# Optimization experiments

Hardware: AMD Instinct MI355X
Metric: run time of the kernel (lower is better)

Reference implementation:

```python
import jax, jax.numpy as jnp
import numpy as np

ALPHA = 0.5
PATH_LEN = 7  # 1 start entity + 3 (module, entity) hops
NUM_ENTITIES = 200000
EMBED = 128
NUM_MOD = 64
HIDDEN = 512
OUT_DIM = 64
BATCH = 8192


def setup_inputs() -> dict:
    key = jax.random.key(0)
    ks = jax.random.split(key, 8)
    stdv = 1.0 / np.sqrt(EMBED)
    return {
        "entity_embeds": jax.random.normal(ks[0], (NUM_ENTITIES, EMBED), jnp.float32) * 0.05,
        "W_mods": jax.random.uniform(ks[1], (NUM_MOD, EMBED, EMBED), jnp.float32, -stdv, stdv),
        "W1": jax.random.normal(ks[2], (HIDDEN, EMBED), jnp.float32) * stdv,
        "b1": jax.random.normal(ks[3], (HIDDEN,), jnp.float32) * 0.01,
        "W2": jax.random.normal(ks[4], (OUT_DIM, HIDDEN), jnp.float32) * (1.0 / np.sqrt(HIDDEN)),
        "b2": jax.random.normal(ks[5], (OUT_DIM,), jnp.float32) * 0.01,
        "entity_ids": jax.random.randint(ks[6], (BATCH, 4), 0, NUM_ENTITIES, jnp.int64 if jax.config.jax_enable_x64 else jnp.int32),
        "module_ids": jax.random.randint(ks[7], (BATCH, 3), 0, NUM_MOD, jnp.int64 if jax.config.jax_enable_x64 else jnp.int32),
    }


def reference(entity_embeds, W_mods, W1, b1, W2, b2, entity_ids, module_ids):
    # Batched version of ModuleNet.forward over a batch of fixed-length-7 paths.
    x = entity_embeds[entity_ids[:, 0]]  # [B, E] start entity embedding
    bias = x
    for h in range(3):  # hops over (module_id, entity_id) pairs
        Wm = W_mods[module_ids[:, h]]          # [B, E, E] per-row weight gather
        bias = entity_embeds[entity_ids[:, h + 1]]  # [B, E]
        x = jax.nn.relu(jnp.einsum('boi,bi->bo', Wm, x) + bias)
    w = 1.0 / (PATH_LEN * ALPHA)
    out = (1.0 - w) * bias + w * x  # [B, E]
    # classifier: Linear -> ReLU -> Linear
    h1 = jax.nn.relu(out @ W1.T + b1)
    logits = h1 @ W2.T + b2  # [B, OUT_DIM]
    return logits
```

## Files before the change

kernel.cpp:

```cpp
#include <hip/hip_runtime.h>

namespace {

typedef short bf16x8 __attribute__((ext_vector_type(8)));
typedef float f32x4 __attribute__((ext_vector_type(4)));

constexpr int BATCH = 8192;
constexpr int NMOD  = 64;
constexpr int CAP   = 256;
constexpr int CSTR  = 16;
constexpr float WB  = 1.0f / (7.0f * 0.5f);

constexpr size_t OFF_WHI = 0;
constexpr size_t OFF_WLO = 524288;
constexpr size_t OFF_XH0 = 1048576;
constexpr size_t OFF_XL0 = 1572864;
constexpr size_t OFF_XH1 = 2097152;
constexpr size_t OFF_XL1 = 2621440;
constexpr size_t OFF_W1H = 3145728;
constexpr size_t OFF_W1L = 3178496;
constexpr size_t OFF_W2H = 3211264;
constexpr size_t OFF_W2L = 3227648;
constexpr size_t OFF_CNT = 3244032;
constexpr size_t OFF_BKT = 3247104;

__device__ __forceinline__ ushort f2bf(float x) {
  unsigned u = __builtin_bit_cast(unsigned, x);
  u += 0x7FFFu + ((u >> 16) & 1u);
  return (ushort)(u >> 16);
}
__device__ __forceinline__ float bf2f(ushort h) {
  return __builtin_bit_cast(float, ((unsigned)h) << 16);
}
__device__ __forceinline__ void cvt8(const float* v, bf16x8& hi, bf16x8& lo) {
#pragma unroll
  for (int j = 0; j < 8; ++j) {
    const float x = v[j];
    const ushort h = f2bf(x);
    hi[j] = (short)h;
    lo[j] = (short)f2bf(x - bf2f(h));
  }
}

__global__ __launch_bounds__(256) void k_prep(const float* __restrict__ Wm,
                                              const float* __restrict__ W1,
                                              const float* __restrict__ W2,
                                              const int* __restrict__ mids,
                                              float* __restrict__ ws) {
  const int bx = blockIdx.x;
  const int tid = threadIdx.x;
  if (bx < 560) {
    const float* src;
    ushort *dh, *dl;
    size_t i8;
    if (bx < 512) {
      src = Wm; dh = (ushort*)(ws + OFF_WHI); dl = (ushort*)(ws + OFF_WLO);
      i8 = (size_t)bx * 256 + tid;
    } else if (bx < 544) {
      src = W1; dh = (ushort*)(ws + OFF_W1H); dl = (ushort*)(ws + OFF_W1L);
      i8 = (size_t)(bx - 512) * 256 + tid;
    } else {
      src = W2; dh = (ushort*)(ws + OFF_W2H); dl = (ushort*)(ws + OFF_W2L);
      i8 = (size_t)(bx - 544) * 256 + tid;
    }
    float v[8];
    *(float4*)&v[0] = *(const float4*)&src[i8 * 8];
    *(float4*)&v[4] = *(const float4*)&src[i8 * 8 + 4];
    bf16x8 hi, lo;
    cvt8(v, hi, lo);
    *(bf16x8*)&dh[i8 * 8] = hi;
    *(bf16x8*)&dl[i8 * 8] = lo;
  } else {
    const int idx = (bx - 560) * 256 + tid;
    if (idx < BATCH * 3) {
      const int b = idx / 3, h = idx - b * 3;
      const int m = mids[idx];
      int* cnt = (int*)(ws + OFF_CNT);
      int* bkt = (int*)(ws + OFF_BKT);
      const int pos = atomicAdd(&cnt[(h * NMOD + m) * CSTR], 1);
      bkt[(h * NMOD + m) * CAP + pos] = b;
    }
  }
}

template <int HOP>
__global__ __launch_bounds__(256, 2) void k_hop(const float* __restrict__ E,
                                                const int* __restrict__ eids,
                                                float* __restrict__ ws) {
  const int m = blockIdx.x >> 2, sl = blockIdx.x & 3;
  const int cn = ((const int*)(ws + OFF_CNT))[(HOP * NMOD + m) * CSTR];
  const int r0 = sl * 64;
  if (r0 >= cn) return;
  const int nr = min(64, cn - r0);

  __shared__ ushort wh[128 * 72];
  __shared__ ushort wl[128 * 72];
  __shared__ int rows[64], esrc[64], ebia[64];

  const int tid = threadIdx.x;
  const ushort* WhiG = (const ushort*)(ws + OFF_WHI) + (size_t)m * 16384;
  const ushort* WloG = (const ushort*)(ws + OFF_WLO) + (size_t)m * 16384;
  const int* bkt = (const int*)(ws + OFF_BKT) + (HOP * NMOD + m) * CAP + r0;
  const ushort* XHp = (const ushort*)(ws + (HOP == 2 ? OFF_XH1 : OFF_XH0));
  const ushort* XLp = (const ushort*)(ws + (HOP == 2 ? OFF_XL1 : OFF_XL0));
  ushort* XHn = (ushort*)(ws + (HOP == 1 ? OFF_XH1 : OFF_XH0));
  ushort* XLn = (ushort*)(ws + (HOP == 1 ? OFF_XL1 : OFF_XL0));

  if (tid < 64) {
    const int b = bkt[tid < nr ? tid : 0];
    rows[tid] = b;
    esrc[tid] = (HOP == 0) ? eids[b * 4] : b;
    ebia[tid] = eids[b * 4 + HOP + 1];
  }

  const int w = tid >> 6, l = tid & 63;
  const int lg = l >> 4, lr = l & 15;
  const int g0 = (w & 1) * 2, f0 = (w >> 1) * 4;

  f32x4 acc[2][4] = {};

#pragma unroll
  for (int p = 0; p < 2; ++p) {
    __syncthreads();
    for (int e = tid; e < 128 * 8; e += 256) {
      const int c = e >> 3, s = e & 7;
      *(bf16x8*)&wh[c * 72 + s * 8] =
          *(const bf16x8*)&WhiG[(size_t)c * 128 + p * 64 + s * 8];
      *(bf16x8*)&wl[c * 72 + s * 8] =
          *(const bf16x8*)&WloG[(size_t)c * 128 + p * 64 + s * 8];
    }
    __syncthreads();

    bf16x8 ah[2][2], al[2][2];
#pragma unroll
    for (int g = 0; g < 2; ++g) {
      const int row = (g0 + g) * 16 + lr;
#pragma unroll
      for (int s = 0; s < 2; ++s) {
        const int k0 = p * 64 + s * 32 + lg * 8;
        if (HOP == 0) {
          const float* sp = E + (size_t)esrc[row] * 128;
          float v[8];
          *(float4*)&v[0] = *(const float4*)&sp[k0];
          *(float4*)&v[4] = *(const float4*)&sp[k0 + 4];
          cvt8(v, ah[g][s], al[g][s]);
        } else {
          const size_t xo = (size_t)esrc[row] * 128 + k0;
          ah[g][s] = *(const bf16x8*)&XHp[xo];
          al[g][s] = *(const bf16x8*)&XLp[xo];
        }
      }
    }

#pragma unroll
    for (int f = 0; f < 4; ++f) {
      const int c = (f0 + f) * 16 + lr;
      bf16x8 bh[2], bl[2];
#pragma unroll
      for (int s = 0; s < 2; ++s) {
        bh[s] = *(const bf16x8*)&wh[c * 72 + s * 32 + lg * 8];
        bl[s] = *(const bf16x8*)&wl[c * 72 + s * 32 + lg * 8];
      }
#pragma unroll
      for (int g = 0; g < 2; ++g) {
#pragma unroll
        for (int s = 0; s < 2; ++s) {
          acc[g][f] = __builtin_amdgcn_mfma_f32_16x16x32_bf16(
              ah[g][s], bh[s], acc[g][f], 0, 0, 0);
          acc[g][f] = __builtin_amdgcn_mfma_f32_16x16x32_bf16(
              al[g][s], bh[s], acc[g][f], 0, 0, 0);
          acc[g][f] = __builtin_amdgcn_mfma_f32_16x16x32_bf16(
              ah[g][s], bl[s], acc[g][f], 0, 0, 0);
        }
      }
    }
  }

#pragma unroll
  for (int g = 0; g < 2; ++g) {
#pragma unroll
    for (int q = 0; q < 4; ++q) {
      const int row = (g0 + g) * 16 + lg * 4 + q;
      if (row < nr) {
        const int b = rows[row];
        const float* bp = E + (size_t)ebia[row] * 128;
        const size_t ob = (size_t)b * 128;
#pragma unroll
        for (int f = 0; f < 4; ++f) {
          const int col = (f0 + f) * 16 + lr;
          const float bias = bp[col];
          float v = fmaxf(acc[g][f][q] + bias, 0.f);
          if (HOP == 2) v = (1.f - WB) * bias + WB * v;
          const ushort h = f2bf(v);
          XHn[ob + col] = h;
          XLn[ob + col] = f2bf(v - bf2f(h));
        }
      }
    }
  }
}

constexpr int HSTR = 520;
__global__ __launch_bounds__(256, 2) void k_mlp(const float* __restrict__ b1,
                                                const float* __restrict__ b2,
                                                float* __restrict__ ws,
                                                float* __restrict__ out) {
  __shared__ ushort hh[16 * HSTR];
  __shared__ ushort hl[16 * HSTR];
  const int tid = threadIdx.x;
  const int row0 = blockIdx.x * 16;
  const ushort* XH = (const ushort*)(ws + OFF_XH0);
  const ushort* XL = (const ushort*)(ws + OFF_XL0);
  const ushort* W1H = (const ushort*)(ws + OFF_W1H);
  const ushort* W1L = (const ushort*)(ws + OFF_W1L);
  const ushort* W2H = (const ushort*)(ws + OFF_W2H);
  const ushort* W2L = (const ushort*)(ws + OFF_W2L);

  const int w = tid >> 6, l = tid & 63;
  const int lg = l >> 4, lr = l & 15;

  bf16x8 ah[4], al[4];
#pragma unroll
  for (int s = 0; s < 4; ++s) {
    const size_t xo = (size_t)(row0 + lr) * 128 + s * 32 + lg * 8;
    ah[s] = *(const bf16x8*)&XH[xo];
    al[s] = *(const bf16x8*)&XL[xo];
  }
  f32x4 acc[8] = {};
#pragma unroll
  for (int f = 0; f < 8; ++f) {
    const int c = w * 128 + f * 16 + lr;
#pragma unroll
    for (int s = 0; s < 4; ++s) {
      const size_t wo = (size_t)c * 128 + s * 32 + lg * 8;
      const bf16x8 bh = *(const bf16x8*)&W1H[wo];
      const bf16x8 bl = *(const bf16x8*)&W1L[wo];
      acc[f] = __builtin_amdgcn_mfma_f32_16x16x32_bf16(ah[s], bh, acc[f], 0, 0, 0);
      acc[f] = __builtin_amdgcn_mfma_f32_16x16x32_bf16(al[s], bh, acc[f], 0, 0, 0);
      acc[f] = __builtin_amdgcn_mfma_f32_16x16x32_bf16(ah[s], bl, acc[f], 0, 0, 0);
    }
  }
#pragma unroll
  for (int f = 0; f < 8; ++f) {
    const int c = w * 128 + f * 16 + lr;
    const float bb = b1[c];
#pragma unroll
    for (int q = 0; q < 4; ++q) {
      const int r = lg * 4 + q;
      const float v = fmaxf(acc[f][q] + bb, 0.f);
      const ushort h = f2bf(v);
      hh[r * HSTR + c] = h;
      hl[r * HSTR + c] = f2bf(v - bf2f(h));
    }
  }
  __syncthreads();

  f32x4 acc2 = {};
#pragma unroll 4
  for (int s = 0; s < 16; ++s) {
    const size_t wo = (size_t)(w * 16 + lr) * 512 + s * 32 + lg * 8;
    const bf16x8 a2h = *(const bf16x8*)&W2H[wo];
    const bf16x8 a2l = *(const bf16x8*)&W2L[wo];
    const int ko = s * 32 + lg * 8;
    const bf16x8 b2h = *(const bf16x8*)&hh[lr * HSTR + ko];
    const bf16x8 b2l = *(const bf16x8*)&hl[lr * HSTR + ko];
    acc2 = __builtin_amdgcn_mfma_f32_16x16x32_bf16(a2h, b2h, acc2, 0, 0, 0);
    acc2 = __builtin_amdgcn_mfma_f32_16x16x32_bf16(a2l, b2h, acc2, 0, 0, 0);
    acc2 = __builtin_amdgcn_mfma_f32_16x16x32_bf16(a2h, b2l, acc2, 0, 0, 0);
  }
  const float4 bb2 = *(const float4*)&b2[w * 16 + lg * 4];
  float4 o;
  o.x = acc2[0] + bb2.x;
  o.y = acc2[1] + bb2.y;
  o.z = acc2[2] + bb2.z;
  o.w = acc2[3] + bb2.w;
  *(float4*)&out[(size_t)(row0 + lr) * 64 + w * 16 + lg * 4] = o;
}

}

extern "C" void kernel_launch(void* const* d_in, const int* in_sizes, int n_in,
                              void* d_out, int out_size, void* d_ws,
                              size_t ws_size, hipStream_t stream) {
  const float* E  = (const float*)d_in[0];
  const float* Wm = (const float*)d_in[1];
  const float* W1 = (const float*)d_in[2];
  const float* b1 = (const float*)d_in[3];
  const float* W2 = (const float*)d_in[4];
  const float* b2 = (const float*)d_in[5];
  const int* eids = (const int*)d_in[6];
  const int* mids = (const int*)d_in[7];
  float* out = (float*)d_out;
  float* ws = (float*)d_ws;

  (void)hipMemsetAsync((char*)d_ws + OFF_CNT * sizeof(float), 0,
                       192 * CSTR * sizeof(int), stream);
  k_prep<<<dim3(656), dim3(256), 0, stream>>>(Wm, W1, W2, mids, ws);
  k_hop<0><<<dim3(256), dim3(256), 0, stream>>>(E, eids, ws);
  k_hop<1><<<dim3(256), dim3(256), 0, stream>>>(E, eids, ws);
  k_hop<2><<<dim3(256), dim3(256), 0, stream>>>(E, eids, ws);
  k_mlp<<<dim3(512), dim3(256), 0, stream>>>(b1, b2, ws, out);
}
```

Baseline: 80.18 us.

## Convert module weights on the fly in hop kernels, replace atomic bucketing with ballot compaction

The separate pre-pass that split all 64 module weight matrices into bf16 hi/lo workspace copies is removed. Each hop block now reads fp32 weights directly and converts them into shared memory, which avoids a 4 MB round trip at the cost of repeating the conversion per block and per hop. Bucketing of batch rows by module now uses one block per (hop, module) with ballot/popcount compaction instead of global atomics, which also removes the memset and gives deterministic ordering. Hop blocks now cover 32 rows instead of 64, doubling the grid to 512 blocks for better occupancy but loading the weights twice as often.

```diff
diff --git a/kernel.cpp b/kernel.cpp
--- a/kernel.cpp
+++ b/kernel.cpp
@@ -11,18 +11,16 @@
 constexpr int CSTR  = 16;
 constexpr float WB  = 1.0f / (7.0f * 0.5f);
 
-constexpr size_t OFF_WHI = 0;
-constexpr size_t OFF_WLO = 524288;
-constexpr size_t OFF_XH0 = 1048576;
-constexpr size_t OFF_XL0 = 1572864;
-constexpr size_t OFF_XH1 = 2097152;
-constexpr size_t OFF_XL1 = 2621440;
-constexpr size_t OFF_W1H = 3145728;
-constexpr size_t OFF_W1L = 3178496;
-constexpr size_t OFF_W2H = 3211264;
-constexpr size_t OFF_W2L = 3227648;
-constexpr size_t OFF_CNT = 3244032;
-constexpr size_t OFF_BKT = 3247104;
+constexpr size_t OFF_XH0 = 0;
+constexpr size_t OFF_XL0 = 524288;
+constexpr size_t OFF_XH1 = 1048576;
+constexpr size_t OFF_XL1 = 1572864;
+constexpr size_t OFF_W1H = 2097152;
+constexpr size_t OFF_W1L = 2129920;
+constexpr size_t OFF_W2H = 2162688;
+constexpr size_t OFF_W2L = 2179072;
+constexpr size_t OFF_CNT = 2195456;
+constexpr size_t OFF_BKT = 2198528;
 
 __device__ __forceinline__ ushort f2bf(float x) {
   unsigned u = __builtin_bit_cast(unsigned, x);
@@ -42,26 +40,23 @@
   }
 }
 
-__global__ __launch_bounds__(256) void k_prep(const float* __restrict__ Wm,
-                                              const float* __restrict__ W1,
+__global__ __launch_bounds__(256) void k_prep(const float* __restrict__ W1,
                                               const float* __restrict__ W2,
                                               const int* __restrict__ mids,
                                               float* __restrict__ ws) {
+  __shared__ int wsum[4];
   const int bx = blockIdx.x;
   const int tid = threadIdx.x;
-  if (bx < 560) {
+  if (bx < 48) {
     const float* src;
     ushort *dh, *dl;
     size_t i8;
-    if (bx < 512) {
-      src = Wm; dh = (ushort*)(ws + OFF_WHI); dl = (ushort*)(ws + OFF_WLO);
+    if (bx < 32) {
+      src = W1; dh = (ushort*)(ws + OFF_W1H); dl = (ushort*)(ws + OFF_W1L);
       i8 = (size_t)bx * 256 + tid;
-    } else if (bx < 544) {
-      src = W1; dh = (ushort*)(ws + OFF_W1H); dl = (ushort*)(ws + OFF_W1L);
-      i8 = (size_t)(bx - 512) * 256 + tid;
     } else {
       src = W2; dh = (ushort*)(ws + OFF_W2H); dl = (ushort*)(ws + OFF_W2L);
-      i8 = (size_t)(bx - 544) * 256 + tid;
+      i8 = (size_t)(bx - 32) * 256 + tid;
     }
     float v[8];
     *(float4*)&v[0] = *(const float4*)&src[i8 * 8];
@@ -71,42 +66,55 @@
     *(bf16x8*)&dh[i8 * 8] = hi;
     *(bf16x8*)&dl[i8 * 8] = lo;
   } else {
-    const int idx = (bx - 560) * 256 + tid;
-    if (idx < BATCH * 3) {
-      const int b = idx / 3, h = idx - b * 3;
-      const int m = mids[idx];
-      int* cnt = (int*)(ws + OFF_CNT);
-      int* bkt = (int*)(ws + OFF_BKT);
-      const int pos = atomicAdd(&cnt[(h * NMOD + m) * CSTR], 1);
-      bkt[(h * NMOD + m) * CAP + pos] = b;
-    }
+    const int hm = bx - 48;
+    const int h = hm >> 6, m = hm & 63;
+    int* cnt = (int*)(ws + OFF_CNT);
+    int* bkt = (int*)(ws + OFF_BKT) + hm * CAP;
+    const int wv = tid >> 6, ln = tid & 63;
+    int count = 0;
+    for (int it = 0; it < BATCH / 256; ++it) {
+      const int b = it * 256 + tid;
+      const bool hit = (mids[b * 3 + h] == m);
+      const unsigned long long mask = __ballot(hit);
+      const int pre = __popcll(mask & ((1ull << ln) - 1ull));
+      if (ln == 0) wsum[wv] = __popcll(mask);
+      __syncthreads();
+      int wbase = count;
+#pragma unroll
+      for (int u = 0; u < 4; ++u)
+        if (u < wv) wbase += wsum[u];
+      if (hit) bkt[wbase + pre] = b;
+      count += wsum[0] + wsum[1] + wsum[2] + wsum[3];
+      __syncthreads();
+    }
+    if (tid == 0) cnt[hm * CSTR] = count;
   }
 }
 
 template <int HOP>
 __global__ __launch_bounds__(256, 2) void k_hop(const float* __restrict__ E,
+                                                const float* __restrict__ Wm,
                                                 const int* __restrict__ eids,
                                                 float* __restrict__ ws) {
-  const int m = blockIdx.x >> 2, sl = blockIdx.x & 3;
+  const int m = blockIdx.x >> 3, sl = blockIdx.x & 7;
   const int cn = ((const int*)(ws + OFF_CNT))[(HOP * NMOD + m) * CSTR];
-  const int r0 = sl * 64;
+  const int r0 = sl * 32;
   if (r0 >= cn) return;
-  const int nr = min(64, cn - r0);
+  const int nr = min(32, cn - r0);
 
   __shared__ ushort wh[128 * 72];
   __shared__ ushort wl[128 * 72];
-  __shared__ int rows[64], esrc[64], ebia[64];
+  __shared__ int rows[32], esrc[32], ebia[32];
 
   const int tid = threadIdx.x;
-  const ushort* WhiG = (const ushort*)(ws + OFF_WHI) + (size_t)m * 16384;
-  const ushort* WloG = (const ushort*)(ws + OFF_WLO) + (size_t)m * 16384;
+  const float* WmG = Wm + (size_t)m * 16384;
   const int* bkt = (const int*)(ws + OFF_BKT) + (HOP * NMOD + m) * CAP + r0;
   const ushort* XHp = (const ushort*)(ws + (HOP == 2 ? OFF_XH1 : OFF_XH0));
   const ushort* XLp = (const ushort*)(ws + (HOP == 2 ? OFF_XL1 : OFF_XL0));
   ushort* XHn = (ushort*)(ws + (HOP == 1 ? OFF_XH1 : OFF_XH0));
   ushort* XLn = (ushort*)(ws + (HOP == 1 ? OFF_XL1 : OFF_XL0));
 
-  if (tid < 64) {
+  if (tid < 32) {
     const int b = bkt[tid < nr ? tid : 0];
     rows[tid] = b;
     esrc[tid] = (HOP == 0) ? eids[b * 4] : b;
@@ -115,86 +123,74 @@
 
   const int w = tid >> 6, l = tid & 63;
   const int lg = l >> 4, lr = l & 15;
-  const int g0 = (w & 1) * 2, f0 = (w >> 1) * 4;
-
-  f32x4 acc[2][4] = {};
+  const int g = w & 1, f0 = (w >> 1) * 4;
+  const int row = g * 16 + lr;
+
+  f32x4 acc[4] = {};
 
 #pragma unroll
   for (int p = 0; p < 2; ++p) {
     __syncthreads();
     for (int e = tid; e < 128 * 8; e += 256) {
       const int c = e >> 3, s = e & 7;
-      *(bf16x8*)&wh[c * 72 + s * 8] =
-          *(const bf16x8*)&WhiG[(size_t)c * 128 + p * 64 + s * 8];
-      *(bf16x8*)&wl[c * 72 + s * 8] =
-          *(const bf16x8*)&WloG[(size_t)c * 128 + p * 64 + s * 8];
+      float v[8];
+      const float* sp = &WmG[(size_t)c * 128 + p * 64 + s * 8];
+      *(float4*)&v[0] = *(const float4*)&sp[0];
+      *(float4*)&v[4] = *(const float4*)&sp[4];
+      bf16x8 hi, lo;
+      cvt8(v, hi, lo);
+      *(bf16x8*)&wh[c * 72 + s * 8] = hi;
+      *(bf16x8*)&wl[c * 72 + s * 8] = lo;
     }
     __syncthreads();
 
-    bf16x8 ah[2][2], al[2][2];
-#pragma unroll
-    for (int g = 0; g < 2; ++g) {
-      const int row = (g0 + g) * 16 + lr;
-#pragma unroll
-      for (int s = 0; s < 2; ++s) {
-        const int k0 = p * 64 + s * 32 + lg * 8;
-        if (HOP == 0) {
-          const float* sp = E + (size_t)esrc[row] * 128;
-          float v[8];
-          *(float4*)&v[0] = *(const float4*)&sp[k0];
-          *(float4*)&v[4] = *(const float4*)&sp[k0 + 4];
-          cvt8(v, ah[g][s], al[g][s]);
-        } else {
-          const size_t xo = (size_t)esrc[row] * 128 + k0;
-          ah[g][s] = *(const bf16x8*)&XHp[xo];
-          al[g][s] = *(const bf16x8*)&XLp[xo];
-        }
+    bf16x8 ah[2], al[2];
+#pragma unroll
+    for (int s = 0; s < 2; ++s) {
+      const int k0 = p * 64 + s * 32 + lg * 8;
+      if (HOP == 0) {
+        const float* sp = E + (size_t)esrc[row] * 128;
+        float v[8];
+        *(float4*)&v[0] = *(const float4*)&sp[k0];
+        *(float4*)&v[4] = *(const float4*)&sp[k0 + 4];
+        cvt8(v, ah[s], al[s]);
+      } else {
+        const size_t xo = (size_t)esrc[row] * 128 + k0;
+        ah[s] = *(const bf16x8*)&XHp[xo];
+        al[s] = *(const bf16x8*)&XLp[xo];
       }
     }
 
 #pragma unroll
     for (int f = 0; f < 4; ++f) {
       const int c = (f0 + f) * 16 + lr;
-      bf16x8 bh[2], bl[2];
 #pragma unroll
       for (int s = 0; s < 2; ++s) {
-        bh[s] = *(const bf16x8*)&wh[c * 72 + s * 32 + lg * 8];
-        bl[s] = *(const bf16x8*)&wl[c * 72 + s * 32 + lg * 8];
+        const bf16x8 bh = *(const bf16x8*)&wh[c * 72 + s * 32 + lg * 8];
+        const bf16x8 bl = *(const bf16x8*)&wl[c * 72 + s * 32 + lg * 8];
+        acc[f] = __builtin_amdgcn_mfma_f32_16x16x32_bf16(ah[s], bh, acc[f], 0, 0, 0);
+        acc[f] = __builtin_amdgcn_mfma_f32_16x16x32_bf16(al[s], bh, acc[f], 0, 0, 0);
+        acc[f] = __builtin_amdgcn_mfma_f32_16x16x32_bf16(ah[s], bl, acc[f], 0, 0, 0);
       }
-#pragma unroll
-      for (int g = 0; g < 2; ++g) {
-#pragma unroll
-        for (int s = 0; s < 2; ++s) {
-          acc[g][f] = __builtin_amdgcn_mfma_f32_16x16x32_bf16(
-              ah[g][s], bh[s], acc[g][f], 0, 0, 0);
-          acc[g][f] = __builtin_amdgcn_mfma_f32_16x16x32_bf16(
-              al[g][s], bh[s], acc[g][f], 0, 0, 0);
-          acc[g][f] = __builtin_amdgcn_mfma_f32_16x16x32_bf16(
-              ah[g][s], bl[s], acc[g][f], 0, 0, 0);
-        }
-      }
-    }
-  }
-
-#pragma unroll
-  for (int g = 0; g < 2; ++g) {
-#pragma unroll
-    for (int q = 0; q < 4; ++q) {
-      const int row = (g0 + g) * 16 + lg * 4 + q;
-      if (row < nr) {
-        const int b = rows[row];
-        const float* bp = E + (size_t)ebia[row] * 128;
-        const size_t ob = (size_t)b * 128;
-#pragma unroll
-        for (int f = 0; f < 4; ++f) {
-          const int col = (f0 + f) * 16 + lr;
-          const float bias = bp[col];
-          float v = fmaxf(acc[g][f][q] + bias, 0.f);
-          if (HOP == 2) v = (1.f - WB) * bias + WB * v;
-          const ushort h = f2bf(v);
-          XHn[ob + col] = h;
-          XLn[ob + col] = f2bf(v - bf2f(h));
-        }
+    }
+  }
+
+#pragma unroll
+  for (int q = 0; q < 4; ++q) {
+    const int orow = g * 16 + lg * 4 + q;
+    if (orow < nr) {
+      const int b = rows[orow];
+      const float* bp = E + (size_t)ebia[orow] * 128;
+      const size_t ob = (size_t)b * 128;
+#pragma unroll
+      for (int f = 0; f < 4; ++f) {
+        const int col = (f0 + f) * 16 + lr;
+        const float bias = bp[col];
+        float v = fmaxf(acc[f][q] + bias, 0.f);
+        if (HOP == 2) v = (1.f - WB) * bias + WB * v;
+        const ushort h = f2bf(v);
+        XHn[ob + col] = h;
+        XLn[ob + col] = f2bf(v - bf2f(h));
       }
     }
   }
@@ -293,11 +289,9 @@
   float* out = (float*)d_out;
   float* ws = (float*)d_ws;
 
-  (void)hipMemsetAsync((char*)d_ws + OFF_CNT * sizeof(float), 0,
-                       192 * CSTR * sizeof(int), stream);
-  k_prep<<<dim3(656), dim3(256), 0, stream>>>(Wm, W1, W2, mids, ws);
-  k_hop<0><<<dim3(256), dim3(256), 0, stream>>>(E, eids, ws);
-  k_hop<1><<<dim3(256), dim3(256), 0, stream>>>(E, eids, ws);
-  k_hop<2><<<dim3(256), dim3(256), 0, stream>>>(E, eids, ws);
+  k_prep<<<dim3(240), dim3(256), 0, stream>>>(W1, W2, mids, ws);
+  k_hop<0><<<dim3(512), dim3(256), 0, stream>>>(E, Wm, eids, ws);
+  k_hop<1><<<dim3(512), dim3(256), 0, stream>>>(E, Wm, eids, ws);
+  k_hop<2><<<dim3(512), dim3(256), 0, stream>>>(E, Wm, eids, ws);
   k_mlp<<<dim3(512), dim3(256), 0, stream>>>(b1, b2, ws, out);
 }
```

Result: slower. 82.25 us (+2.6%).
